# Kernel tuning notes

Hardware: AMD Instinct MI355X
Metric: run time of the kernel (lower is better)

The kernel has to match this reference:

```python
import jax, jax.numpy as jnp
import numpy as np

NUM_CLASSES = 80
BBOX_W, OBJ_W, CLS_W = 2.0, 1.0, 0.5
ALPHA, GAMMA = 0.25, 2.0


def setup_inputs() -> dict:
    key = jax.random.key(0)
    ks = jax.random.split(key, 8)
    B, T = 32, 64
    return {
        "cls_p4": jax.random.normal(ks[0], (B, 1 + NUM_CLASSES, 80, 80), jnp.float32),
        "reg_p4": jax.random.normal(ks[1], (B, 4, 80, 80), jnp.float32),
        "cls_p5": jax.random.normal(ks[2], (B, 1 + NUM_CLASSES, 40, 40), jnp.float32),
        "reg_p5": jax.random.normal(ks[3], (B, 4, 40, 40), jnp.float32),
        "t4_cls": jax.random.randint(ks[4], (B, T), 0, NUM_CLASSES, jnp.int32),
        "t4_box": jax.random.uniform(ks[5], (B, T, 4), jnp.float32),
        "t4_mask": jnp.ones((B, T), jnp.float32),
        "t5_cls": jax.random.randint(ks[6], (B, T), 0, NUM_CLASSES, jnp.int32),
        "t5_box": jax.random.uniform(ks[7], (B, T, 4), jnp.float32),
        "t5_mask": jnp.ones((B, T), jnp.float32),
    }


def _bce_logits(x, t):
    # stable BCEWithLogits: log(1+e^x) - x*t
    return jnp.logaddexp(0.0, x) - x * t


def _scale_loss(cls_p, reg_p, cls_ids, box, mask):
    B, C, H, W = cls_p.shape
    tx = box[..., 0] * W  # [B,T]
    ty = box[..., 1] * H
    tw = box[..., 2] * W
    th = box[..., 3] * H
    gx = jnp.clip(tx, 0, W - 1).astype(jnp.int32)
    gy = jnp.clip(ty, 0, H - 1).astype(jnp.int32)
    bb = jnp.arange(B)[:, None]  # [B,1] broadcast over T

    # gather per-target reg/cls vectors: [B,T,4] and [B,T,C]
    rv = jnp.transpose(reg_p, (0, 2, 3, 1))[bb, gy, gx]
    cv = jnp.transpose(cls_p, (0, 2, 3, 1))[bb, gy, gx]

    dx = jax.nn.sigmoid(rv[..., 0])
    dy = jax.nn.sigmoid(rv[..., 1])
    dw = jnp.exp(jnp.clip(rv[..., 2], -4.0, 4.0))
    dh = jnp.exp(jnp.clip(rv[..., 3], -4.0, 4.0))
    px = gx.astype(jnp.float32) + dx
    py = gy.astype(jnp.float32) + dy
    pred_box = jnp.stack([px - dw / 2, py - dh / 2, px + dw / 2, py + dh / 2], -1)
    tgt_box = jnp.stack([tx - tw / 2, ty - th / 2, tx + tw / 2, ty + th / 2], -1)

    d = pred_box - tgt_box
    sl1 = jnp.where(jnp.abs(d) < 1.0, 0.5 * d * d, jnp.abs(d) - 0.5).mean(-1)  # [B,T]
    lb = (sl1 * mask).sum()

    # objectness loss at target cells (target = 1)
    obj_t = cv[..., 0]
    lo = (jax.nn.softplus(-obj_t) * mask).sum()

    # focal classification loss
    onehot = jax.nn.one_hot(cls_ids, C - 1, dtype=cls_p.dtype)  # [B,T,NC]
    logits = cv[..., 1:]
    bce = _bce_logits(logits, onehot)
    p = jax.nn.sigmoid(logits)
    pt = p * onehot + (1.0 - p) * (1.0 - onehot)
    focal = (ALPHA * (1.0 - pt) ** GAMMA * bce).mean(-1)  # [B,T]
    lc = (focal * mask).sum()

    n = mask.sum()

    # background objectness: cells not hit by any valid target
    obj_map = jnp.zeros((B, H, W), cls_p.dtype).at[bb, gy, gx].max(mask)
    bg = obj_map == 0
    bg_cnt = bg.sum()
    bce_bg = jnp.where(bg, jax.nn.softplus(cls_p[:, 0]), 0.0).sum()
    lo = lo + 0.05 * jnp.where(bg_cnt > 0, bce_bg / jnp.maximum(bg_cnt, 1), 0.0)
    return lb, lo, lc, n


def reference(cls_p4, reg_p4, cls_p5, reg_p5,
              t4_cls, t4_box, t4_mask, t5_cls, t5_box, t5_mask):
    lb4, lo4, lc4, n4 = _scale_loss(cls_p4, reg_p4, t4_cls, t4_box, t4_mask)
    lb5, lo5, lc5, n5 = _scale_loss(cls_p5, reg_p5, t5_cls, t5_box, t5_mask)
    lb, lo, lc, n = lb4 + lb5, lo4 + lo5, lc4 + lc5, n4 + n5
    lb = jnp.where(n > 0, lb / jnp.maximum(n, 1), lb)
    lc = jnp.where(n > 0, lc / jnp.maximum(n, 1), lc)
    lo = lo / jnp.maximum(n, 1.0)
    total = BBOX_W * lb + OBJ_W * lo + CLS_W * lc
    return total
```

## Files before the change

### kernel.cpp

```cpp
#include <hip/hip_runtime.h>
#include <math.h>

#define NUM_CLASSES 80
#define C_CH (NUM_CLASSES + 1)
#define MAX_T 128

__device__ __forceinline__ float softplusf(float x) {
    return fmaxf(x, 0.f) + log1pf(expf(-fabsf(x)));
}
__device__ __forceinline__ float sigmoidf_(float x) {
    return 1.f / (1.f + expf(-x));
}


__global__ void fused_kernel(
    const float* __restrict__ cls_p4, const float* __restrict__ reg_p4,
    const float* __restrict__ cls_p5, const float* __restrict__ reg_p5,
    const int* __restrict__ t4_cls, const float* __restrict__ t4_box, const float* __restrict__ t4_mask,
    const int* __restrict__ t5_cls, const float* __restrict__ t5_box, const float* __restrict__ t5_mask,
    float* __restrict__ bgpart, float* __restrict__ tpart, float* __restrict__ occpart,
    int B, int T, int nbg4, int nbg5, int nTblk)
{
    const int tid  = threadIdx.x;
    const int wave = tid >> 6;
    const int lane = tid & 63;
    const int nbg  = nbg4 + nbg5;
    const int BT   = B * T;

    if ((int)blockIdx.x < nbg) {
        const int blk = blockIdx.x;
        float sp = 0.f;
        if (blk < nbg4) {
            int b = blk / 25, j = blk - b * 25;
            int cell = j * 256 + tid;
            sp = softplusf(cls_p4[(size_t)b * (C_CH * 6400) + cell]);
        } else {
            int o = blk - nbg4;
            int b = o / 7, j = o - b * 7;
            int cell = j * 256 + tid;
            if (cell < 1600)
                sp = softplusf(cls_p5[(size_t)b * (C_CH * 1600) + cell]);
        }
        for (int off = 32; off > 0; off >>= 1) sp += __shfl_down(sp, off, 64);
        __shared__ float ss[4];
        if (lane == 0) ss[wave] = sp;
        __syncthreads();
        if (tid == 0) bgpart[blockIdx.x] = ss[0] + ss[1] + ss[2] + ss[3];
        return;
    }

    if ((int)blockIdx.x < nbg + nTblk) {
        const int tg = ((int)blockIdx.x - nbg) * 4 + wave;
        float lb = 0.f, lo = 0.f, lcv = 0.f, msum = 0.f;

        if (tg < 2 * BT) {
            const int scale = (tg >= BT) ? 1 : 0;
            const int ti = scale ? tg - BT : tg;
            const int b = ti / T;

            const float* cls_p; const float* reg_p; const int* tc; const float* tb_; const float* tm;
            int H, W;
            if (!scale) { cls_p = cls_p4; reg_p = reg_p4; tc = t4_cls; tb_ = t4_box; tm = t4_mask; H = 80; W = 80; }
            else        { cls_p = cls_p5; reg_p = reg_p5; tc = t5_cls; tb_ = t5_box; tm = t5_mask; H = 40; W = 40; }
            const int HW = H * W;

            const float mask = tm[ti];
            const int   cid  = tc[ti];
            const float bx0 = tb_[ti * 4 + 0], bx1 = tb_[ti * 4 + 1];
            const float bx2 = tb_[ti * 4 + 2], bx3 = tb_[ti * 4 + 3];

            const float tx = bx0 * (float)W, ty = bx1 * (float)H;
            const float tw = bx2 * (float)W, th = bx3 * (float)H;
            const int gx = (int)fminf(fmaxf(tx, 0.f), (float)(W - 1));
            const int gy = (int)fminf(fmaxf(ty, 0.f), (float)(H - 1));
            const int cell = gy * W + gx;

            const float* cvbase = cls_p + (size_t)b * C_CH * HW + cell;

            float rvq = 0.f;
            if (lane < 4) rvq = reg_p[(size_t)(b * 4 + lane) * HW + cell];
            float objq = (lane == 0) ? cvbase[0] : 0.f;

            float fsum = 0.f;
            for (int c = lane; c < NUM_CLASSES; c += 64) {
                float x   = cvbase[(size_t)(c + 1) * HW];
                float tgt = (c == cid) ? 1.f : 0.f;
                float bce = softplusf(x) - x * tgt;
                float p   = sigmoidf_(x);
                float pt  = p * tgt + (1.f - p) * (1.f - tgt);
                float om  = 1.f - pt;
                fsum += 0.25f * om * om * bce;
            }
            for (int off = 32; off > 0; off >>= 1) fsum += __shfl_down(fsum, off, 64);

            float rv0 = __shfl(rvq, 0, 64), rv1 = __shfl(rvq, 1, 64);
            float rv2 = __shfl(rvq, 2, 64), rv3 = __shfl(rvq, 3, 64);

            if (lane == 0) {
                lcv = (fsum * (1.f / (float)NUM_CLASSES)) * mask;
                lo  = softplusf(-objq) * mask;

                float dx = sigmoidf_(rv0), dy = sigmoidf_(rv1);
                float dw = expf(fminf(fmaxf(rv2, -4.f), 4.f));
                float dh = expf(fminf(fmaxf(rv3, -4.f), 4.f));
                float px = (float)gx + dx, py = (float)gy + dy;
                float pb0 = px - dw * 0.5f, pb1 = py - dh * 0.5f, pb2 = px + dw * 0.5f, pb3 = py + dh * 0.5f;
                float tb0 = tx - tw * 0.5f, tb1 = ty - th * 0.5f, tb2 = tx + tw * 0.5f, tb3 = ty + th * 0.5f;
                float s = 0.f, d, a;
                d = pb0 - tb0; a = fabsf(d); s += (a < 1.f) ? 0.5f * d * d : a - 0.5f;
                d = pb1 - tb1; a = fabsf(d); s += (a < 1.f) ? 0.5f * d * d : a - 0.5f;
                d = pb2 - tb2; a = fabsf(d); s += (a < 1.f) ? 0.5f * d * d : a - 0.5f;
                d = pb3 - tb3; a = fabsf(d); s += (a < 1.f) ? 0.5f * d * d : a - 0.5f;
                lb = (s * 0.25f) * mask;
                msum = mask;
            }
        }

        __shared__ float s4[4][4];
        if (lane == 0) { s4[wave][0] = lb; s4[wave][1] = lo; s4[wave][2] = lcv; s4[wave][3] = msum; }
        __syncthreads();
        if (tid < 4) {
            float v = s4[0][tid] + s4[1][tid] + s4[2][tid] + s4[3][tid];
            tpart[((int)blockIdx.x - nbg) * 4 + tid] = v;
        }
        return;
    }

    {
        __shared__ unsigned int cells[4][MAX_T];
        const int p = ((int)blockIdx.x - nbg - nTblk) * 4 + wave;
        float osp = 0.f, ocnt = 0.f;
        bool valid_pair = (p < 2 * B) && (T <= MAX_T);
        int scale = 0, b = 0;
        const float* tb_ = nullptr; const float* tm = nullptr;
        int W = 80, HW = 6400;
        if (valid_pair) {
            scale = p / B; b = p - scale * B;
            tb_ = scale ? t5_box : t4_box;
            tm  = scale ? t5_mask : t4_mask;
            W = scale ? 40 : 80; HW = W * W;
            for (int i = lane; i < T; i += 64) {
                const int ti = b * T + i;
                unsigned int cellv = 0xFFFFFFFFu;
                if (tm[ti] > 0.f) {
                    const float tx = tb_[ti * 4 + 0] * (float)W;
                    const float ty = tb_[ti * 4 + 1] * (float)W;
                    const int gx = (int)fminf(fmaxf(tx, 0.f), (float)(W - 1));
                    const int gy = (int)fminf(fmaxf(ty, 0.f), (float)(W - 1));
                    cellv = (unsigned)(gy * W + gx);
                }
                cells[wave][i] = cellv;
            }
        }
        __syncthreads();
        if (valid_pair) {
            const float* cls_p = scale ? cls_p5 : cls_p4;
            for (int i = lane; i < T; i += 64) {
                unsigned int cv = cells[wave][i];
                if (cv != 0xFFFFFFFFu) {
                    bool first = true;
                    for (int j = 0; j < i; j++)
                        if (cells[wave][j] == cv) { first = false; break; }
                    if (first) {
                        osp  += softplusf(cls_p[(size_t)b * C_CH * HW + (int)cv]);
                        ocnt += 1.f;
                    }
                }
            }
        }
        for (int off = 32; off > 0; off >>= 1) {
            osp  += __shfl_down(osp,  off, 64);
            ocnt += __shfl_down(ocnt, off, 64);
        }
        if (lane == 0 && p < 2 * B) {
            occpart[p * 2]     = osp;
            occpart[p * 2 + 1] = ocnt;
        }
    }
}

__global__ void __launch_bounds__(256) final_kernel(
    const float* __restrict__ bgpart, int nbg4, int nbg5,
    const float* __restrict__ tpart, int nTblk,
    const float* __restrict__ occpart,
    int B, float* __restrict__ out)
{
    const int tid = threadIdx.x;
    float lb = 0.f, lo = 0.f, lc = 0.f, n = 0.f;
    float bg4 = 0.f, bg5 = 0.f, o4 = 0.f, c4 = 0.f, o5 = 0.f, c5 = 0.f;

    for (int i = tid; i < nTblk; i += 256) {
        lb += tpart[i * 4 + 0]; lo += tpart[i * 4 + 1];
        lc += tpart[i * 4 + 2]; n  += tpart[i * 4 + 3];
    }
    for (int i = tid; i < nbg4; i += 256) bg4 += bgpart[i];
    for (int i = tid; i < nbg5; i += 256) bg5 += bgpart[nbg4 + i];
    for (int p = tid; p < 2 * B; p += 256) {
        if (p < B) { o4 += occpart[p * 2]; c4 += occpart[p * 2 + 1]; }
        else       { o5 += occpart[p * 2]; c5 += occpart[p * 2 + 1]; }
    }

    __shared__ float red[4][10];
    float vals[10] = { lb, lo, lc, n, bg4, bg5, o4, c4, o5, c5 };
    #pragma unroll
    for (int k = 0; k < 10; k++) {
        float v = vals[k];
        for (int off = 32; off > 0; off >>= 1) v += __shfl_down(v, off, 64);
        vals[k] = v;
    }
    if ((tid & 63) == 0) {
        #pragma unroll
        for (int k = 0; k < 10; k++) red[tid >> 6][k] = vals[k];
    }
    __syncthreads();
    if (tid == 0) {
        float t[10];
        #pragma unroll
        for (int k = 0; k < 10; k++)
            t[k] = red[0][k] + red[1][k] + red[2][k] + red[3][k];

        float lbt = t[0], lot = t[1], lct = t[2], nt = t[3];
        float bce_bg4 = t[4] - t[6];
        float bce_bg5 = t[5] - t[8];
        float cnt4 = (float)(B * 6400) - t[7];
        float cnt5 = (float)(B * 1600) - t[9];
        lot += 0.05f * ((cnt4 > 0.f) ? bce_bg4 / fmaxf(cnt4, 1.f) : 0.f);
        lot += 0.05f * ((cnt5 > 0.f) ? bce_bg5 / fmaxf(cnt5, 1.f) : 0.f);
        float nd = fmaxf(nt, 1.f);
        if (nt > 0.f) { lbt /= nd; lct /= nd; }
        lot /= fmaxf(nt, 1.f);
        out[0] = 2.0f * lbt + 1.0f * lot + 0.5f * lct;
    }
}

extern "C" void kernel_launch(void* const* d_in, const int* in_sizes, int n_in,
                              void* d_out, int out_size, void* d_ws, size_t ws_size,
                              hipStream_t stream) {
    const float* cls_p4 = (const float*)d_in[0];
    const float* reg_p4 = (const float*)d_in[1];
    const float* cls_p5 = (const float*)d_in[2];
    const float* reg_p5 = (const float*)d_in[3];
    const int*   t4_cls = (const int*)d_in[4];
    const float* t4_box = (const float*)d_in[5];
    const float* t4_mask= (const float*)d_in[6];
    const int*   t5_cls = (const int*)d_in[7];
    const float* t5_box = (const float*)d_in[8];
    const float* t5_mask= (const float*)d_in[9];

    const int B = in_sizes[0] / (C_CH * 6400);
    const int T = in_sizes[4] / B;
    const int BT = B * T;

    const int nbg4  = B * 25;
    const int nbg5  = B * 7;
    const int nTblk = (2 * BT + 3) / 4;
    const int ndblk = (2 * B + 3) / 4;

    float* bgpart  = (float*)d_ws;
    float* tpart   = bgpart + (nbg4 + nbg5);
    float* occpart = tpart + (size_t)nTblk * 4;

    fused_kernel<<<nbg4 + nbg5 + nTblk + ndblk, 256, 0, stream>>>(
        cls_p4, reg_p4, cls_p5, reg_p5,
        t4_cls, t4_box, t4_mask, t5_cls, t5_box, t5_mask,
        bgpart, tpart, occpart, B, T, nbg4, nbg5, nTblk);

    final_kernel<<<1, 256, 0, stream>>>(bgpart, nbg4, nbg5, tpart, nTblk,
                                        occpart, B, (float*)d_out);
}
```

Measured before the change: 126.8 us.

## Merge final reduction into single kernel via atomics and last-block finalization

Replaces the two-kernel scheme with one kernel that accumulates partial sums through global atomics, and has the last block to finish (tracked by an atomic counter) compute the final loss. The second launch goes away, at the cost of a memset before the kernel. Background blocks now handle one full batch image each and read it with float4 vector loads. Target blocks process two targets per wave and issue their gathers ahead of the math. This trades launch overhead for atomic contention and a threadfence-based completion protocol, and float atomics make the summation order nondeterministic.

```diff
diff --git a/kernel.cpp b/kernel.cpp
--- a/kernel.cpp
+++ b/kernel.cpp
@@ -13,141 +13,170 @@
 }
 
 
-__global__ void fused_kernel(
+__global__ void __launch_bounds__(256) mono_kernel(
     const float* __restrict__ cls_p4, const float* __restrict__ reg_p4,
     const float* __restrict__ cls_p5, const float* __restrict__ reg_p5,
     const int* __restrict__ t4_cls, const float* __restrict__ t4_box, const float* __restrict__ t4_mask,
     const int* __restrict__ t5_cls, const float* __restrict__ t5_box, const float* __restrict__ t5_mask,
-    float* __restrict__ bgpart, float* __restrict__ tpart, float* __restrict__ occpart,
-    int B, int T, int nbg4, int nbg5, int nTblk)
+    float* __restrict__ acc, unsigned int* __restrict__ counter,
+    int B, int T, int nT, int nblk_total, float* __restrict__ out)
 {
     const int tid  = threadIdx.x;
     const int wave = tid >> 6;
     const int lane = tid & 63;
-    const int nbg  = nbg4 + nbg5;
+    const int blk  = (int)blockIdx.x;
     const int BT   = B * T;
 
-    if ((int)blockIdx.x < nbg) {
-        const int blk = blockIdx.x;
-        float sp = 0.f;
-        if (blk < nbg4) {
-            int b = blk / 25, j = blk - b * 25;
-            int cell = j * 256 + tid;
-            sp = softplusf(cls_p4[(size_t)b * (C_CH * 6400) + cell]);
-        } else {
-            int o = blk - nbg4;
-            int b = o / 7, j = o - b * 7;
-            int cell = j * 256 + tid;
-            if (cell < 1600)
-                sp = softplusf(cls_p5[(size_t)b * (C_CH * 1600) + cell]);
-        }
-        for (int off = 32; off > 0; off >>= 1) sp += __shfl_down(sp, off, 64);
-        __shared__ float ss[4];
-        if (lane == 0) ss[wave] = sp;
-        __syncthreads();
-        if (tid == 0) bgpart[blockIdx.x] = ss[0] + ss[1] + ss[2] + ss[3];
-        return;
-    }
-
-    if ((int)blockIdx.x < nbg + nTblk) {
-        const int tg = ((int)blockIdx.x - nbg) * 4 + wave;
-        float lb = 0.f, lo = 0.f, lcv = 0.f, msum = 0.f;
-
-        if (tg < 2 * BT) {
-            const int scale = (tg >= BT) ? 1 : 0;
-            const int ti = scale ? tg - BT : tg;
-            const int b = ti / T;
-
-            const float* cls_p; const float* reg_p; const int* tc; const float* tb_; const float* tm;
-            int H, W;
-            if (!scale) { cls_p = cls_p4; reg_p = reg_p4; tc = t4_cls; tb_ = t4_box; tm = t4_mask; H = 80; W = 80; }
-            else        { cls_p = cls_p5; reg_p = reg_p5; tc = t5_cls; tb_ = t5_box; tm = t5_mask; H = 40; W = 40; }
-            const int HW = H * W;
-
-            const float mask = tm[ti];
-            const int   cid  = tc[ti];
-            const float bx0 = tb_[ti * 4 + 0], bx1 = tb_[ti * 4 + 1];
-            const float bx2 = tb_[ti * 4 + 2], bx3 = tb_[ti * 4 + 3];
-
-            const float tx = bx0 * (float)W, ty = bx1 * (float)H;
-            const float tw = bx2 * (float)W, th = bx3 * (float)H;
-            const int gx = (int)fminf(fmaxf(tx, 0.f), (float)(W - 1));
-            const int gy = (int)fminf(fmaxf(ty, 0.f), (float)(H - 1));
-            const int cell = gy * W + gx;
-
-            const float* cvbase = cls_p + (size_t)b * C_CH * HW + cell;
-
-            float rvq = 0.f;
-            if (lane < 4) rvq = reg_p[(size_t)(b * 4 + lane) * HW + cell];
-            float objq = (lane == 0) ? cvbase[0] : 0.f;
-
+    __shared__ float s4[4][4];
+
+    if (blk < B) {
+        const float* base = cls_p4 + (size_t)blk * (C_CH * 6400);
+        const float4* v4 = (const float4*)base;
+        float s = 0.f;
+        #pragma unroll
+        for (int k = 0; k < 6; k++) {
+            float4 x = v4[k * 256 + tid];
+            s += softplusf(x.x) + softplusf(x.y) + softplusf(x.z) + softplusf(x.w);
+        }
+        s += softplusf(base[6144 + tid]);
+        for (int off = 32; off > 0; off >>= 1) s += __shfl_down(s, off, 64);
+        if (lane == 0) s4[wave][0] = s;
+        __syncthreads();
+        if (tid == 0) atomicAdd(&acc[4], s4[0][0] + s4[1][0] + s4[2][0] + s4[3][0]);
+    } else if (blk < 2 * B) {
+        const int b = blk - B;
+        const float* base = cls_p5 + (size_t)b * (C_CH * 1600);
+        const float4* v4 = (const float4*)base;
+        float4 x = v4[tid];
+        float s = softplusf(x.x) + softplusf(x.y) + softplusf(x.z) + softplusf(x.w);
+        if (tid < 144) {
+            float4 y = v4[256 + tid];
+            s += softplusf(y.x) + softplusf(y.y) + softplusf(y.z) + softplusf(y.w);
+        }
+        for (int off = 32; off > 0; off >>= 1) s += __shfl_down(s, off, 64);
+        if (lane == 0) s4[wave][0] = s;
+        __syncthreads();
+        if (tid == 0) atomicAdd(&acc[5], s4[0][0] + s4[1][0] + s4[2][0] + s4[3][0]);
+    } else if (blk < 2 * B + nT) {
+        const int pw = (blk - 2 * B) * 4 + wave;
+        float lbS = 0.f, loS = 0.f, lcS = 0.f, nS = 0.f;
+
+        bool   ok[2];
+        float  mask[2], tx[2], ty[2], tw[2], th[2];
+        int    cid[2], gx[2], gy[2], HWv[2];
+        const float* cvb[2]; const float* rgb[2];
+
+        #pragma unroll
+        for (int k = 0; k < 2; k++) {
+            const int tg = pw * 2 + k;
+            ok[k] = (tg < 2 * BT);
+            cvb[k] = nullptr; rgb[k] = nullptr;
+            if (ok[k]) {
+                const int scale = (tg >= BT) ? 1 : 0;
+                const int ti = scale ? tg - BT : tg;
+                const int b = ti / T;
+                const float* cls_p = scale ? cls_p5 : cls_p4;
+                const float* reg_p = scale ? reg_p5 : reg_p4;
+                const int*   tc    = scale ? t5_cls : t4_cls;
+                const float* tb_   = scale ? t5_box : t4_box;
+                const float* tm    = scale ? t5_mask : t4_mask;
+                const int W = scale ? 40 : 80;
+                const int HW = W * W;
+                mask[k] = tm[ti];
+                cid[k]  = tc[ti];
+                tx[k] = tb_[ti * 4 + 0] * (float)W;
+                ty[k] = tb_[ti * 4 + 1] * (float)W;
+                tw[k] = tb_[ti * 4 + 2] * (float)W;
+                th[k] = tb_[ti * 4 + 3] * (float)W;
+                gx[k] = (int)fminf(fmaxf(tx[k], 0.f), (float)(W - 1));
+                gy[k] = (int)fminf(fmaxf(ty[k], 0.f), (float)(W - 1));
+                const int cell = gy[k] * W + gx[k];
+                HWv[k] = HW;
+                cvb[k] = cls_p + (size_t)b * C_CH * HW + cell;
+                rgb[k] = reg_p + (size_t)(b * 4) * HW + cell;
+            }
+        }
+
+        float x0[2], x1[2], rvq[2], objq[2];
+        #pragma unroll
+        for (int k = 0; k < 2; k++) {
+            x0[k] = ok[k] ? cvb[k][(size_t)(lane + 1) * HWv[k]] : 0.f;
+            x1[k] = (ok[k] && lane < NUM_CLASSES - 64) ? cvb[k][(size_t)(lane + 65) * HWv[k]] : 0.f;
+            rvq[k]  = (ok[k] && lane < 4) ? rgb[k][(size_t)lane * HWv[k]] : 0.f;
+            objq[k] = (ok[k] && lane == 0) ? cvb[k][0] : 0.f;
+        }
+
+        #pragma unroll
+        for (int k = 0; k < 2; k++) {
             float fsum = 0.f;
-            for (int c = lane; c < NUM_CLASSES; c += 64) {
-                float x   = cvbase[(size_t)(c + 1) * HW];
-                float tgt = (c == cid) ? 1.f : 0.f;
+            {
+                float x = x0[k];
+                float tgt = (lane == cid[k]) ? 1.f : 0.f;
                 float bce = softplusf(x) - x * tgt;
-                float p   = sigmoidf_(x);
-                float pt  = p * tgt + (1.f - p) * (1.f - tgt);
-                float om  = 1.f - pt;
+                float p = sigmoidf_(x);
+                float pt = p * tgt + (1.f - p) * (1.f - tgt);
+                float om = 1.f - pt;
+                if (lane < NUM_CLASSES) fsum += 0.25f * om * om * bce;
+            }
+            if (lane < NUM_CLASSES - 64) {
+                float x = x1[k];
+                float tgt = (lane + 64 == cid[k]) ? 1.f : 0.f;
+                float bce = softplusf(x) - x * tgt;
+                float p = sigmoidf_(x);
+                float pt = p * tgt + (1.f - p) * (1.f - tgt);
+                float om = 1.f - pt;
                 fsum += 0.25f * om * om * bce;
             }
             for (int off = 32; off > 0; off >>= 1) fsum += __shfl_down(fsum, off, 64);
 
-            float rv0 = __shfl(rvq, 0, 64), rv1 = __shfl(rvq, 1, 64);
-            float rv2 = __shfl(rvq, 2, 64), rv3 = __shfl(rvq, 3, 64);
-
-            if (lane == 0) {
-                lcv = (fsum * (1.f / (float)NUM_CLASSES)) * mask;
-                lo  = softplusf(-objq) * mask;
+            float rv0 = __shfl(rvq[k], 0, 64), rv1 = __shfl(rvq[k], 1, 64);
+            float rv2 = __shfl(rvq[k], 2, 64), rv3 = __shfl(rvq[k], 3, 64);
+
+            if (lane == 0 && ok[k]) {
+                const float m = mask[k];
+                lcS += (fsum * (1.f / (float)NUM_CLASSES)) * m;
+                loS += softplusf(-objq[k]) * m;
 
                 float dx = sigmoidf_(rv0), dy = sigmoidf_(rv1);
                 float dw = expf(fminf(fmaxf(rv2, -4.f), 4.f));
                 float dh = expf(fminf(fmaxf(rv3, -4.f), 4.f));
-                float px = (float)gx + dx, py = (float)gy + dy;
-                float pb0 = px - dw * 0.5f, pb1 = py - dh * 0.5f, pb2 = px + dw * 0.5f, pb3 = py + dh * 0.5f;
-                float tb0 = tx - tw * 0.5f, tb1 = ty - th * 0.5f, tb2 = tx + tw * 0.5f, tb3 = ty + th * 0.5f;
-                float s = 0.f, d, a;
-                d = pb0 - tb0; a = fabsf(d); s += (a < 1.f) ? 0.5f * d * d : a - 0.5f;
-                d = pb1 - tb1; a = fabsf(d); s += (a < 1.f) ? 0.5f * d * d : a - 0.5f;
-                d = pb2 - tb2; a = fabsf(d); s += (a < 1.f) ? 0.5f * d * d : a - 0.5f;
-                d = pb3 - tb3; a = fabsf(d); s += (a < 1.f) ? 0.5f * d * d : a - 0.5f;
-                lb = (s * 0.25f) * mask;
-                msum = mask;
-            }
-        }
-
-        __shared__ float s4[4][4];
-        if (lane == 0) { s4[wave][0] = lb; s4[wave][1] = lo; s4[wave][2] = lcv; s4[wave][3] = msum; }
+                float px = (float)gx[k] + dx, py = (float)gy[k] + dy;
+                float d, a, s = 0.f;
+                d = (px - dw * 0.5f) - (tx[k] - tw[k] * 0.5f); a = fabsf(d); s += (a < 1.f) ? 0.5f * d * d : a - 0.5f;
+                d = (py - dh * 0.5f) - (ty[k] - th[k] * 0.5f); a = fabsf(d); s += (a < 1.f) ? 0.5f * d * d : a - 0.5f;
+                d = (px + dw * 0.5f) - (tx[k] + tw[k] * 0.5f); a = fabsf(d); s += (a < 1.f) ? 0.5f * d * d : a - 0.5f;
+                d = (py + dh * 0.5f) - (ty[k] + th[k] * 0.5f); a = fabsf(d); s += (a < 1.f) ? 0.5f * d * d : a - 0.5f;
+                lbS += (s * 0.25f) * m;
+                nS  += m;
+            }
+        }
+
+        if (lane == 0) { s4[wave][0] = lbS; s4[wave][1] = loS; s4[wave][2] = lcS; s4[wave][3] = nS; }
         __syncthreads();
         if (tid < 4) {
             float v = s4[0][tid] + s4[1][tid] + s4[2][tid] + s4[3][tid];
-            tpart[((int)blockIdx.x - nbg) * 4 + tid] = v;
-        }
-        return;
-    }
-
-    {
+            atomicAdd(&acc[tid], v);
+        }
+    } else {
         __shared__ unsigned int cells[4][MAX_T];
-        const int p = ((int)blockIdx.x - nbg - nTblk) * 4 + wave;
+        const int p = (blk - 2 * B - nT) * 4 + wave;
         float osp = 0.f, ocnt = 0.f;
-        bool valid_pair = (p < 2 * B) && (T <= MAX_T);
-        int scale = 0, b = 0;
-        const float* tb_ = nullptr; const float* tm = nullptr;
-        int W = 80, HW = 6400;
+        const bool valid_pair = (p < 2 * B) && (T <= MAX_T);
+        int scale = 0, b = 0, W = 80, HW = 6400;
         if (valid_pair) {
             scale = p / B; b = p - scale * B;
-            tb_ = scale ? t5_box : t4_box;
-            tm  = scale ? t5_mask : t4_mask;
+            const float* tb_ = scale ? t5_box : t4_box;
+            const float* tm  = scale ? t5_mask : t4_mask;
             W = scale ? 40 : 80; HW = W * W;
             for (int i = lane; i < T; i += 64) {
                 const int ti = b * T + i;
                 unsigned int cellv = 0xFFFFFFFFu;
                 if (tm[ti] > 0.f) {
-                    const float tx = tb_[ti * 4 + 0] * (float)W;
-                    const float ty = tb_[ti * 4 + 1] * (float)W;
-                    const int gx = (int)fminf(fmaxf(tx, 0.f), (float)(W - 1));
-                    const int gy = (int)fminf(fmaxf(ty, 0.f), (float)(W - 1));
-                    cellv = (unsigned)(gy * W + gx);
+                    const float txx = tb_[ti * 4 + 0] * (float)W;
+                    const float tyy = tb_[ti * 4 + 1] * (float)W;
+                    const int gxx = (int)fminf(fmaxf(txx, 0.f), (float)(W - 1));
+                    const int gyy = (int)fminf(fmaxf(tyy, 0.f), (float)(W - 1));
+                    cellv = (unsigned)(gyy * W + gxx);
                 }
                 cells[wave][i] = cellv;
             }
@@ -173,63 +202,33 @@
             ocnt += __shfl_down(ocnt, off, 64);
         }
         if (lane == 0 && p < 2 * B) {
-            occpart[p * 2]     = osp;
-            occpart[p * 2 + 1] = ocnt;
-        }
+            atomicAdd(&acc[6 + 2 * scale], osp);
+            atomicAdd(&acc[7 + 2 * scale], ocnt);
+        }
+        __syncthreads();
     }
-}
-
-__global__ void __launch_bounds__(256) final_kernel(
-    const float* __restrict__ bgpart, int nbg4, int nbg5,
-    const float* __restrict__ tpart, int nTblk,
-    const float* __restrict__ occpart,
-    int B, float* __restrict__ out)
-{
-    const int tid = threadIdx.x;
-    float lb = 0.f, lo = 0.f, lc = 0.f, n = 0.f;
-    float bg4 = 0.f, bg5 = 0.f, o4 = 0.f, c4 = 0.f, o5 = 0.f, c5 = 0.f;
-
-    for (int i = tid; i < nTblk; i += 256) {
-        lb += tpart[i * 4 + 0]; lo += tpart[i * 4 + 1];
-        lc += tpart[i * 4 + 2]; n  += tpart[i * 4 + 3];
-    }
-    for (int i = tid; i < nbg4; i += 256) bg4 += bgpart[i];
-    for (int i = tid; i < nbg5; i += 256) bg5 += bgpart[nbg4 + i];
-    for (int p = tid; p < 2 * B; p += 256) {
-        if (p < B) { o4 += occpart[p * 2]; c4 += occpart[p * 2 + 1]; }
-        else       { o5 += occpart[p * 2]; c5 += occpart[p * 2 + 1]; }
-    }
-
-    __shared__ float red[4][10];
-    float vals[10] = { lb, lo, lc, n, bg4, bg5, o4, c4, o5, c5 };
-    #pragma unroll
-    for (int k = 0; k < 10; k++) {
-        float v = vals[k];
-        for (int off = 32; off > 0; off >>= 1) v += __shfl_down(v, off, 64);
-        vals[k] = v;
-    }
-    if ((tid & 63) == 0) {
-        #pragma unroll
-        for (int k = 0; k < 10; k++) red[tid >> 6][k] = vals[k];
-    }
+
     __syncthreads();
     if (tid == 0) {
-        float t[10];
-        #pragma unroll
-        for (int k = 0; k < 10; k++)
-            t[k] = red[0][k] + red[1][k] + red[2][k] + red[3][k];
-
-        float lbt = t[0], lot = t[1], lct = t[2], nt = t[3];
-        float bce_bg4 = t[4] - t[6];
-        float bce_bg5 = t[5] - t[8];
-        float cnt4 = (float)(B * 6400) - t[7];
-        float cnt5 = (float)(B * 1600) - t[9];
-        lot += 0.05f * ((cnt4 > 0.f) ? bce_bg4 / fmaxf(cnt4, 1.f) : 0.f);
-        lot += 0.05f * ((cnt5 > 0.f) ? bce_bg5 / fmaxf(cnt5, 1.f) : 0.f);
-        float nd = fmaxf(nt, 1.f);
-        if (nt > 0.f) { lbt /= nd; lct /= nd; }
-        lot /= fmaxf(nt, 1.f);
-        out[0] = 2.0f * lbt + 1.0f * lot + 0.5f * lct;
+        __threadfence();
+        unsigned int old = atomicAdd(counter, 1u);
+        if (old == (unsigned int)(nblk_total - 1)) {
+            __threadfence();
+            float t[10];
+            #pragma unroll
+            for (int k = 0; k < 10; k++) t[k] = atomicAdd(&acc[k], 0.f);
+            float lbt = t[0], lot = t[1], lct = t[2], nt = t[3];
+            float bce_bg4 = t[4] - t[6];
+            float bce_bg5 = t[5] - t[8];
+            float cnt4 = (float)(B * 6400) - t[7];
+            float cnt5 = (float)(B * 1600) - t[9];
+            lot += 0.05f * ((cnt4 > 0.f) ? bce_bg4 / fmaxf(cnt4, 1.f) : 0.f);
+            lot += 0.05f * ((cnt5 > 0.f) ? bce_bg5 / fmaxf(cnt5, 1.f) : 0.f);
+            float nd = fmaxf(nt, 1.f);
+            if (nt > 0.f) { lbt /= nd; lct /= nd; }
+            lot /= fmaxf(nt, 1.f);
+            out[0] = 2.0f * lbt + 1.0f * lot + 0.5f * lct;
+        }
     }
 }
 
@@ -251,20 +250,17 @@
     const int T = in_sizes[4] / B;
     const int BT = B * T;
 
-    const int nbg4  = B * 25;
-    const int nbg5  = B * 7;
-    const int nTblk = (2 * BT + 3) / 4;
-    const int ndblk = (2 * B + 3) / 4;
-
-    float* bgpart  = (float*)d_ws;
-    float* tpart   = bgpart + (nbg4 + nbg5);
-    float* occpart = tpart + (size_t)nTblk * 4;
-
-    fused_kernel<<<nbg4 + nbg5 + nTblk + ndblk, 256, 0, stream>>>(
+    const int nT = (2 * BT + 7) / 8;
+    const int nd = (2 * B + 3) / 4;
+    const int nblk_total = 2 * B + nT + nd;
+
+    float* acc = (float*)d_ws;
+    unsigned int* counter = (unsigned int*)d_ws + 15;
+
+    hipMemsetAsync(d_ws, 0, 64, stream);
+
+    mono_kernel<<<nblk_total, 256, 0, stream>>>(
         cls_p4, reg_p4, cls_p5, reg_p5,
         t4_cls, t4_box, t4_mask, t5_cls, t5_box, t5_mask,
-        bgpart, tpart, occpart, B, T, nbg4, nbg5, nTblk);
-
-    final_kernel<<<1, 256, 0, stream>>>(bgpart, nbg4, nbg5, tpart, nTblk,
-                                        occpart, B, (float*)d_out);
-}
+        acc, counter, B, T, nT, nblk_total, (float*)d_out);
+}
```

Measured after the change: 139.6 us. 1.1x slower.

## Fuse final reduction into main kernel via last-block atomic counter

Applied to the files above, without the earlier changes.

Drops the separate final reduction kernel. Each block now increments a global atomic counter after writing its partials, and the last block to arrive performs the final reduction and writes the output. The goal is to remove the second kernel launch and the gap between launches. In exchange it adds a hipMemsetAsync to reset the counter, plus a threadfence and atomic in every block. The per-target class loop is also unrolled into two explicit loads per lane so they issue early, and tpart is stored column-major.

```diff
diff --git a/kernel.cpp b/kernel.cpp
--- a/kernel.cpp
+++ b/kernel.cpp
@@ -13,22 +13,29 @@
 }
 
 
-__global__ void fused_kernel(
+__global__ void __launch_bounds__(256) mono_kernel(
     const float* __restrict__ cls_p4, const float* __restrict__ reg_p4,
     const float* __restrict__ cls_p5, const float* __restrict__ reg_p5,
     const int* __restrict__ t4_cls, const float* __restrict__ t4_box, const float* __restrict__ t4_mask,
     const int* __restrict__ t5_cls, const float* __restrict__ t5_box, const float* __restrict__ t5_mask,
-    float* __restrict__ bgpart, float* __restrict__ tpart, float* __restrict__ occpart,
-    int B, int T, int nbg4, int nbg5, int nTblk)
+    unsigned int* __restrict__ counter,
+    float* __restrict__ bgpart, float* __restrict__ tpart,
+    float* __restrict__ osp_arr, float* __restrict__ ocnt_arr,
+    int B, int T, int nbg4, int nbg5, int nTblk, int nblk_total,
+    float* __restrict__ out)
 {
     const int tid  = threadIdx.x;
     const int wave = tid >> 6;
     const int lane = tid & 63;
+    const int blk  = (int)blockIdx.x;
     const int nbg  = nbg4 + nbg5;
     const int BT   = B * T;
 
-    if ((int)blockIdx.x < nbg) {
-        const int blk = blockIdx.x;
+    __shared__ float s4[4][4];
+    __shared__ unsigned int cells[4][MAX_T];
+    __shared__ int lastflag;
+
+    if (blk < nbg) {
         float sp = 0.f;
         if (blk < nbg4) {
             int b = blk / 25, j = blk - b * 25;
@@ -42,15 +49,11 @@
                 sp = softplusf(cls_p5[(size_t)b * (C_CH * 1600) + cell]);
         }
         for (int off = 32; off > 0; off >>= 1) sp += __shfl_down(sp, off, 64);
-        __shared__ float ss[4];
-        if (lane == 0) ss[wave] = sp;
-        __syncthreads();
-        if (tid == 0) bgpart[blockIdx.x] = ss[0] + ss[1] + ss[2] + ss[3];
-        return;
-    }
-
-    if ((int)blockIdx.x < nbg + nTblk) {
-        const int tg = ((int)blockIdx.x - nbg) * 4 + wave;
+        if (lane == 0) s4[wave][0] = sp;
+        __syncthreads();
+        if (tid == 0) bgpart[blk] = s4[0][0] + s4[1][0] + s4[2][0] + s4[3][0];
+    } else if (blk < nbg + nTblk) {
+        const int tg = (blk - nbg) * 4 + wave;
         float lb = 0.f, lo = 0.f, lcv = 0.f, msum = 0.f;
 
         if (tg < 2 * BT) {
@@ -58,37 +61,49 @@
             const int ti = scale ? tg - BT : tg;
             const int b = ti / T;
 
-            const float* cls_p; const float* reg_p; const int* tc; const float* tb_; const float* tm;
-            int H, W;
-            if (!scale) { cls_p = cls_p4; reg_p = reg_p4; tc = t4_cls; tb_ = t4_box; tm = t4_mask; H = 80; W = 80; }
-            else        { cls_p = cls_p5; reg_p = reg_p5; tc = t5_cls; tb_ = t5_box; tm = t5_mask; H = 40; W = 40; }
-            const int HW = H * W;
+            const float* cls_p = scale ? cls_p5 : cls_p4;
+            const float* reg_p = scale ? reg_p5 : reg_p4;
+            const int*   tc    = scale ? t5_cls : t4_cls;
+            const float* tb_   = scale ? t5_box : t4_box;
+            const float* tm    = scale ? t5_mask : t4_mask;
+            const int W  = scale ? 40 : 80;
+            const int HW = W * W;
 
             const float mask = tm[ti];
             const int   cid  = tc[ti];
-            const float bx0 = tb_[ti * 4 + 0], bx1 = tb_[ti * 4 + 1];
-            const float bx2 = tb_[ti * 4 + 2], bx3 = tb_[ti * 4 + 3];
-
-            const float tx = bx0 * (float)W, ty = bx1 * (float)H;
-            const float tw = bx2 * (float)W, th = bx3 * (float)H;
+            const float tx = tb_[ti * 4 + 0] * (float)W;
+            const float ty = tb_[ti * 4 + 1] * (float)W;
+            const float tw = tb_[ti * 4 + 2] * (float)W;
+            const float th = tb_[ti * 4 + 3] * (float)W;
             const int gx = (int)fminf(fmaxf(tx, 0.f), (float)(W - 1));
-            const int gy = (int)fminf(fmaxf(ty, 0.f), (float)(H - 1));
+            const int gy = (int)fminf(fmaxf(ty, 0.f), (float)(W - 1));
             const int cell = gy * W + gx;
 
             const float* cvbase = cls_p + (size_t)b * C_CH * HW + cell;
 
-            float rvq = 0.f;
-            if (lane < 4) rvq = reg_p[(size_t)(b * 4 + lane) * HW + cell];
+            float x0 = cvbase[(size_t)(lane + 1) * HW];
+            float x1 = (lane < NUM_CLASSES - 64)
+                         ? cvbase[(size_t)(lane + 65) * HW] : 0.f;
+            float rvq  = (lane < 4) ? reg_p[(size_t)(b * 4 + lane) * HW + cell] : 0.f;
             float objq = (lane == 0) ? cvbase[0] : 0.f;
 
             float fsum = 0.f;
-            for (int c = lane; c < NUM_CLASSES; c += 64) {
-                float x   = cvbase[(size_t)(c + 1) * HW];
-                float tgt = (c == cid) ? 1.f : 0.f;
+            {
+                float x = x0;
+                float tgt = (lane == cid) ? 1.f : 0.f;
                 float bce = softplusf(x) - x * tgt;
-                float p   = sigmoidf_(x);
-                float pt  = p * tgt + (1.f - p) * (1.f - tgt);
-                float om  = 1.f - pt;
+                float p = sigmoidf_(x);
+                float pt = p * tgt + (1.f - p) * (1.f - tgt);
+                float om = 1.f - pt;
+                fsum += 0.25f * om * om * bce;
+            }
+            if (lane < NUM_CLASSES - 64) {
+                float x = x1;
+                float tgt = (lane + 64 == cid) ? 1.f : 0.f;
+                float bce = softplusf(x) - x * tgt;
+                float p = sigmoidf_(x);
+                float pt = p * tgt + (1.f - p) * (1.f - tgt);
+                float om = 1.f - pt;
                 fsum += 0.25f * om * om * bce;
             }
             for (int off = 32; off > 0; off >>= 1) fsum += __shfl_down(fsum, off, 64);
@@ -104,50 +119,44 @@
                 float dw = expf(fminf(fmaxf(rv2, -4.f), 4.f));
                 float dh = expf(fminf(fmaxf(rv3, -4.f), 4.f));
                 float px = (float)gx + dx, py = (float)gy + dy;
-                float pb0 = px - dw * 0.5f, pb1 = py - dh * 0.5f, pb2 = px + dw * 0.5f, pb3 = py + dh * 0.5f;
-                float tb0 = tx - tw * 0.5f, tb1 = ty - th * 0.5f, tb2 = tx + tw * 0.5f, tb3 = ty + th * 0.5f;
-                float s = 0.f, d, a;
-                d = pb0 - tb0; a = fabsf(d); s += (a < 1.f) ? 0.5f * d * d : a - 0.5f;
-                d = pb1 - tb1; a = fabsf(d); s += (a < 1.f) ? 0.5f * d * d : a - 0.5f;
-                d = pb2 - tb2; a = fabsf(d); s += (a < 1.f) ? 0.5f * d * d : a - 0.5f;
-                d = pb3 - tb3; a = fabsf(d); s += (a < 1.f) ? 0.5f * d * d : a - 0.5f;
+                float d, a, s = 0.f;
+                d = (px - dw * 0.5f) - (tx - tw * 0.5f); a = fabsf(d); s += (a < 1.f) ? 0.5f * d * d : a - 0.5f;
+                d = (py - dh * 0.5f) - (ty - th * 0.5f); a = fabsf(d); s += (a < 1.f) ? 0.5f * d * d : a - 0.5f;
+                d = (px + dw * 0.5f) - (tx + tw * 0.5f); a = fabsf(d); s += (a < 1.f) ? 0.5f * d * d : a - 0.5f;
+                d = (py + dh * 0.5f) - (ty + th * 0.5f); a = fabsf(d); s += (a < 1.f) ? 0.5f * d * d : a - 0.5f;
                 lb = (s * 0.25f) * mask;
                 msum = mask;
             }
         }
 
-        __shared__ float s4[4][4];
         if (lane == 0) { s4[wave][0] = lb; s4[wave][1] = lo; s4[wave][2] = lcv; s4[wave][3] = msum; }
         __syncthreads();
-        if (tid < 4) {
-            float v = s4[0][tid] + s4[1][tid] + s4[2][tid] + s4[3][tid];
-            tpart[((int)blockIdx.x - nbg) * 4 + tid] = v;
-        }
-        return;
-    }
-
-    {
-        __shared__ unsigned int cells[4][MAX_T];
-        const int p = ((int)blockIdx.x - nbg - nTblk) * 4 + wave;
+        if (tid == 0) {
+            const int tb = blk - nbg;
+            #pragma unroll
+            for (int q = 0; q < 4; q++)
+                tpart[q * nTblk + tb] = s4[0][q] + s4[1][q] + s4[2][q] + s4[3][q];
+        }
+    } else {
+        const int pbase = (blk - nbg - nTblk) * 4;
+        const int p = pbase + wave;
         float osp = 0.f, ocnt = 0.f;
-        bool valid_pair = (p < 2 * B) && (T <= MAX_T);
-        int scale = 0, b = 0;
-        const float* tb_ = nullptr; const float* tm = nullptr;
-        int W = 80, HW = 6400;
+        const bool valid_pair = (p < 2 * B) && (T <= MAX_T);
+        int scale = 0, b = 0, W = 80, HW = 6400;
         if (valid_pair) {
             scale = p / B; b = p - scale * B;
-            tb_ = scale ? t5_box : t4_box;
-            tm  = scale ? t5_mask : t4_mask;
+            const float* tb_ = scale ? t5_box : t4_box;
+            const float* tm  = scale ? t5_mask : t4_mask;
             W = scale ? 40 : 80; HW = W * W;
             for (int i = lane; i < T; i += 64) {
                 const int ti = b * T + i;
                 unsigned int cellv = 0xFFFFFFFFu;
                 if (tm[ti] > 0.f) {
-                    const float tx = tb_[ti * 4 + 0] * (float)W;
-                    const float ty = tb_[ti * 4 + 1] * (float)W;
-                    const int gx = (int)fminf(fmaxf(tx, 0.f), (float)(W - 1));
-                    const int gy = (int)fminf(fmaxf(ty, 0.f), (float)(W - 1));
-                    cellv = (unsigned)(gy * W + gx);
+                    const float txx = tb_[ti * 4 + 0] * (float)W;
+                    const float tyy = tb_[ti * 4 + 1] * (float)W;
+                    const int gxx = (int)fminf(fmaxf(txx, 0.f), (float)(W - 1));
+                    const int gyy = (int)fminf(fmaxf(tyy, 0.f), (float)(W - 1));
+                    cellv = (unsigned)(gyy * W + gxx);
                 }
                 cells[wave][i] = cellv;
             }
@@ -172,64 +181,73 @@
             osp  += __shfl_down(osp,  off, 64);
             ocnt += __shfl_down(ocnt, off, 64);
         }
-        if (lane == 0 && p < 2 * B) {
-            occpart[p * 2]     = osp;
-            occpart[p * 2 + 1] = ocnt;
+        if (lane == 0) { s4[wave][0] = osp; s4[wave][1] = ocnt; }
+        __syncthreads();
+        if (tid == 0) {
+            #pragma unroll
+            for (int w = 0; w < 4; w++) {
+                int pp = pbase + w;
+                if (pp < 2 * B) {
+                    osp_arr[pp]  = s4[w][0];
+                    ocnt_arr[pp] = s4[w][1];
+                }
+            }
         }
     }
-}
-
-__global__ void __launch_bounds__(256) final_kernel(
-    const float* __restrict__ bgpart, int nbg4, int nbg5,
-    const float* __restrict__ tpart, int nTblk,
-    const float* __restrict__ occpart,
-    int B, float* __restrict__ out)
-{
-    const int tid = threadIdx.x;
-    float lb = 0.f, lo = 0.f, lc = 0.f, n = 0.f;
-    float bg4 = 0.f, bg5 = 0.f, o4 = 0.f, c4 = 0.f, o5 = 0.f, c5 = 0.f;
-
-    for (int i = tid; i < nTblk; i += 256) {
-        lb += tpart[i * 4 + 0]; lo += tpart[i * 4 + 1];
-        lc += tpart[i * 4 + 2]; n  += tpart[i * 4 + 3];
-    }
-    for (int i = tid; i < nbg4; i += 256) bg4 += bgpart[i];
-    for (int i = tid; i < nbg5; i += 256) bg5 += bgpart[nbg4 + i];
-    for (int p = tid; p < 2 * B; p += 256) {
-        if (p < B) { o4 += occpart[p * 2]; c4 += occpart[p * 2 + 1]; }
-        else       { o5 += occpart[p * 2]; c5 += occpart[p * 2 + 1]; }
-    }
-
-    __shared__ float red[4][10];
-    float vals[10] = { lb, lo, lc, n, bg4, bg5, o4, c4, o5, c5 };
-    #pragma unroll
-    for (int k = 0; k < 10; k++) {
-        float v = vals[k];
-        for (int off = 32; off > 0; off >>= 1) v += __shfl_down(v, off, 64);
-        vals[k] = v;
-    }
-    if ((tid & 63) == 0) {
-        #pragma unroll
-        for (int k = 0; k < 10; k++) red[tid >> 6][k] = vals[k];
+
+    if (tid == 0) {
+        __threadfence();
+        unsigned int old = atomicAdd(counter, 1u);
+        lastflag = (old == (unsigned int)(nblk_total - 1)) ? 1 : 0;
     }
     __syncthreads();
-    if (tid == 0) {
-        float t[10];
+    if (lastflag) {
+        __threadfence();
+
+        float lb = 0.f, lo = 0.f, lc = 0.f, n = 0.f;
+        float bg4 = 0.f, bg5 = 0.f, o4 = 0.f, c4 = 0.f, o5 = 0.f, c5 = 0.f;
+        for (int i = tid; i < nTblk; i += 256) {
+            lb += tpart[i];
+            lo += tpart[nTblk + i];
+            lc += tpart[2 * nTblk + i];
+            n  += tpart[3 * nTblk + i];
+        }
+        for (int i = tid; i < nbg4; i += 256) bg4 += bgpart[i];
+        for (int i = tid; i < nbg5; i += 256) bg5 += bgpart[nbg4 + i];
+        for (int p = tid; p < B; p += 256) { o4 += osp_arr[p];     c4 += ocnt_arr[p]; }
+        for (int p = tid; p < B; p += 256) { o5 += osp_arr[B + p]; c5 += ocnt_arr[B + p]; }
+
+        __shared__ float red[4][10];
+        float vals[10] = { lb, lo, lc, n, bg4, bg5, o4, c4, o5, c5 };
         #pragma unroll
-        for (int k = 0; k < 10; k++)
-            t[k] = red[0][k] + red[1][k] + red[2][k] + red[3][k];
-
-        float lbt = t[0], lot = t[1], lct = t[2], nt = t[3];
-        float bce_bg4 = t[4] - t[6];
-        float bce_bg5 = t[5] - t[8];
-        float cnt4 = (float)(B * 6400) - t[7];
-        float cnt5 = (float)(B * 1600) - t[9];
-        lot += 0.05f * ((cnt4 > 0.f) ? bce_bg4 / fmaxf(cnt4, 1.f) : 0.f);
-        lot += 0.05f * ((cnt5 > 0.f) ? bce_bg5 / fmaxf(cnt5, 1.f) : 0.f);
-        float nd = fmaxf(nt, 1.f);
-        if (nt > 0.f) { lbt /= nd; lct /= nd; }
-        lot /= fmaxf(nt, 1.f);
-        out[0] = 2.0f * lbt + 1.0f * lot + 0.5f * lct;
+        for (int k = 0; k < 10; k++) {
+            float v = vals[k];
+            for (int off = 32; off > 0; off >>= 1) v += __shfl_down(v, off, 64);
+            vals[k] = v;
+        }
+        if (lane == 0) {
+            #pragma unroll
+            for (int k = 0; k < 10; k++) red[wave][k] = vals[k];
+        }
+        __syncthreads();
+        if (tid == 0) {
+            float t[10];
+            #pragma unroll
+            for (int k = 0; k < 10; k++)
+                t[k] = red[0][k] + red[1][k] + red[2][k] + red[3][k];
+
+            float lbt = t[0], lot = t[1], lct = t[2], nt = t[3];
+            float bce_bg4 = t[4] - t[6];
+            float bce_bg5 = t[5] - t[8];
+            float cnt4 = (float)(B * 6400) - t[7];
+            float cnt5 = (float)(B * 1600) - t[9];
+            lot += 0.05f * ((cnt4 > 0.f) ? bce_bg4 / fmaxf(cnt4, 1.f) : 0.f);
+            lot += 0.05f * ((cnt5 > 0.f) ? bce_bg5 / fmaxf(cnt5, 1.f) : 0.f);
+            float nd = fmaxf(nt, 1.f);
+            if (nt > 0.f) { lbt /= nd; lct /= nd; }
+            lot /= fmaxf(nt, 1.f);
+            out[0] = 2.0f * lbt + 1.0f * lot + 0.5f * lct;
+        }
     }
 }
 
@@ -253,18 +271,22 @@
 
     const int nbg4  = B * 25;
     const int nbg5  = B * 7;
+    const int nbg   = nbg4 + nbg5;
     const int nTblk = (2 * BT + 3) / 4;
     const int ndblk = (2 * B + 3) / 4;
-
-    float* bgpart  = (float*)d_ws;
-    float* tpart   = bgpart + (nbg4 + nbg5);
-    float* occpart = tpart + (size_t)nTblk * 4;
-
-    fused_kernel<<<nbg4 + nbg5 + nTblk + ndblk, 256, 0, stream>>>(
+    const int nblk_total = nbg + nTblk + ndblk;
+
+    unsigned int* counter = (unsigned int*)d_ws;
+    float* bgpart  = (float*)d_ws + 16;
+    float* tpart   = bgpart + nbg;
+    float* osp_arr = tpart + (size_t)4 * nTblk;
+    float* ocnt_arr= osp_arr + 2 * B;
+
+    hipMemsetAsync(d_ws, 0, 64, stream);
+
+    mono_kernel<<<nblk_total, 256, 0, stream>>>(
         cls_p4, reg_p4, cls_p5, reg_p5,
         t4_cls, t4_box, t4_mask, t5_cls, t5_box, t5_mask,
-        bgpart, tpart, occpart, B, T, nbg4, nbg5, nTblk);
-
-    final_kernel<<<1, 256, 0, stream>>>(bgpart, nbg4, nbg5, tpart, nTblk,
-                                        occpart, B, (float*)d_out);
-}
+        counter, bgpart, tpart, osp_arr, ocnt_arr,
+        B, T, nbg4, nbg5, nTblk, nblk_total, (float*)d_out);
+}
```

Measured after the change: 194.7 us. 53.5% more time.
